# Kernel optimization log

Hardware: AMD Instinct MI355X
Metric: run time of the kernel (lower is better)

The kernel has to match this reference:

```python
import jax, jax.numpy as jnp
import numpy as np

# sigmas (defaults from the module)
VAR_0, VAR_A, VAR_B = 1.0, 1.0, 0.0

def V_phi(a, b, c):
    # default id_phi: (a, b, c) -> b, where Sigma = [[a, b], [b, c]]
    return b


def setup_inputs() -> dict:
    key = jax.random.key(0)
    kx, ky = jax.random.split(key)
    B, T, D = 128, 1024, 64
    dt = 1.0 / (T - 1)
    scale = np.sqrt(dt / D).astype(np.float32)
    # Brownian-like paths: increments ~ N(0, dt/D) so quadratic variation is O(1)
    # and the multiplicative kernel recurrence stays numerically bounded.
    X = jnp.cumsum(jax.random.normal(kx, (B, T, D), jnp.float32) * scale, axis=1)
    Y = jnp.cumsum(jax.random.normal(ky, (B, T, D), jnp.float32) * scale, axis=1)
    return {"X": X, "Y": Y}


def _kernel_same(dd):
    # dd: (b, T-1) = <dX_t, dX_t> / dt ; returns Kxx: (b, T)
    def step(k, d_t):
        k_new = k + (VAR_A * V_phi(k, k, k) + VAR_B) * d_t
        return k_new, k_new
    k0 = jnp.full((dd.shape[0],), VAR_0, dd.dtype)
    _, ks = jax.lax.scan(step, k0, dd.T)           # ks: (T-1, b)
    return jnp.concatenate([k0[None, :], ks], axis=0).T  # (b, T)


def reference(X, Y):
    bx, T, d = X.shape
    by = Y.shape[0]
    interval = jnp.linspace(0.0, 1.0, T).astype(X.dtype)
    dt = jnp.diff(interval)                         # (T-1,)
    dX = jnp.diff(X, axis=1)                        # (bx, T-1, d)
    dY = jnp.diff(Y, axis=1)                        # (by, T-1, d)

    dXdX = (dX * dX).sum(-1) / dt                   # (bx, T-1)
    dYdY = (dY * dY).sum(-1) / dt                   # (by, T-1)
    dXdY = jnp.einsum('itd,jtd->ijt', dX, dY) / dt  # (bx, by, T-1)

    Kxx = _kernel_same(dXdX)                        # (bx, T)
    Kyy = _kernel_same(dYdY)                        # (by, T)

    def step(k, inp):
        kxx_t, kyy_t, dxy_t = inp                   # (bx,), (by,), (bx, by)
        k_new = k + (VAR_A * V_phi(kxx_t[:, None], k, kyy_t[None, :]) + VAR_B) * dxy_t
        return k_new, k_new

    k0 = jnp.full((bx, by), VAR_0, X.dtype)
    xs = (Kxx[:, :-1].T, Kyy[:, :-1].T, jnp.moveaxis(dXdY, 2, 0))
    _, ks = jax.lax.scan(step, k0, xs)              # (T-1, bx, by)
    K = jnp.concatenate([k0[None], ks], axis=0)     # (T, bx, by)
    return jnp.moveaxis(K, 0, 2)                    # (bx, by, T)
```

## Files before the change

### kernel.cpp

```cpp
#include <hip/hip_runtime.h>
#include <hip/hip_bf16.h>

typedef __attribute__((ext_vector_type(8))) short short8;
typedef __attribute__((ext_vector_type(4))) float floatx4;

constexpr int BX    = 128;
constexpr int TT    = 1024;
constexpr int DDIM  = 64;
constexpr int NPAIR = BX * BX;
constexpr int LCH   = 16;
constexpr int NCH   = TT / LCH;
constexpr float DT_INV = 1023.0f;

__device__ __forceinline__ int sidxE(int row, int k) {
    return row * 64 + ((((k >> 3) ^ (row & 7)) << 3) | (k & 7));
}

__device__ __forceinline__ ushort f2bf(float f) {
    uint u = __builtin_bit_cast(uint, f);
    u += 0x7fffu + ((u >> 16) & 1u);
    return (ushort)(u >> 16);
}

__device__ __forceinline__ void cvt_store(ushort* hiP, ushort* loP, const float* v) {
    uint hw[4], lw[4];
#pragma unroll
    for (int p = 0; p < 4; ++p) {
        const __hip_bfloat162 h = __float22bfloat162_rn(make_float2(v[2 * p], v[2 * p + 1]));
        const float r0 = v[2 * p]     - __bfloat162float(h.x);
        const float r1 = v[2 * p + 1] - __bfloat162float(h.y);
        const __hip_bfloat162 l = __float22bfloat162_rn(make_float2(r0, r1));
        hw[p] = (uint)__bfloat16_as_ushort(h.x) | ((uint)__bfloat16_as_ushort(h.y) << 16);
        lw[p] = (uint)__bfloat16_as_ushort(l.x) | ((uint)__bfloat16_as_ushort(l.y) << 16);
    }
    *(uint4*)hiP = make_uint4(hw[0], hw[1], hw[2], hw[3]);
    *(uint4*)loP = make_uint4(lw[0], lw[1], lw[2], lw[3]);
}

__device__ __forceinline__ void ld8(const float* p, float* dst) {
    const float4 a = *(const float4*)p;
    const float4 b = *(const float4*)(p + 4);
    dst[0] = a.x; dst[1] = a.y; dst[2] = a.z; dst[3] = a.w;
    dst[4] = b.x; dst[5] = b.y; dst[6] = b.z; dst[7] = b.w;
}

template<int WP>
__global__ __launch_bounds__(256, 4) void zchunk_kernel(const float* __restrict__ X,
                                                        const float* __restrict__ Y,
                                                        float* __restrict__ dst,
                                                        float* __restrict__ P)
{
    __shared__ __align__(16) ushort smXhi[2][32 * 64], smXlo[2][32 * 64];
    __shared__ __align__(16) ushort smYhi[2][32 * 64], smYlo[2][32 * 64];

    const int L    = (int)blockIdx.x;
    const int tile = (L >> 3) & 15;
    const int cz   = ((L >> 7) << 3) | (L & 7);
    const int i0 = (tile & 3) * 32;
    const int j0 = (tile >> 2) * 32;
    const int t0 = cz * LCH;
    const int tid  = (int)threadIdx.x;
    const int lane = tid & 63, w = tid >> 6, quad = lane >> 4, l15 = lane & 15;
    const int wr = w >> 1, wc = w & 1;

    const int srow = tid >> 3;
    const int sseg = tid & 7;
    const float* xp = X + (size_t)(i0 + srow) * TT * DDIM + sseg * 8;
    const float* yp = Y + (size_t)(j0 + srow) * TT * DDIM + sseg * 8;

    float cx[8], cy[8];
    float rx[2][8], ry[2][8];
    {
        const int sa = (t0 == 0) ? 0 : (t0 - 1);
        float pvx[8], pvy[8], d[8];
        ld8(xp + (size_t)t0 * DDIM, cx);
        ld8(yp + (size_t)t0 * DDIM, cy);
        ld8(xp + (size_t)sa * DDIM, pvx);
        ld8(yp + (size_t)sa * DDIM, pvy);
        ld8(xp + (size_t)(t0 + 1) * DDIM, rx[1]);
        ld8(yp + (size_t)(t0 + 1) * DDIM, ry[1]);

#pragma unroll
        for (int k = 0; k < 8; ++k) d[k] = cx[k] - pvx[k];
        cvt_store(&smXhi[0][sidxE(srow, sseg * 8)], &smXlo[0][sidxE(srow, sseg * 8)], d);
#pragma unroll
        for (int k = 0; k < 8; ++k) d[k] = cy[k] - pvy[k];
        cvt_store(&smYhi[0][sidxE(srow, sseg * 8)], &smYlo[0][sidxE(srow, sseg * 8)], d);
    }

    float cum[4];
    uint  histP[4][8];
#pragma unroll
    for (int r = 0; r < 4; ++r) cum[r] = 1.f;

    __syncthreads();

#pragma unroll
    for (int h = 0; h < LCH; ++h) {
        const int cur = h & 1;

        if (h + 2 < LCH) {
            const size_t u = (size_t)(t0 + h + 2) * DDIM;
            ld8(xp + u, rx[h & 1]); ld8(yp + u, ry[h & 1]);
        }

        short8 aHi[2], aLo[2];
#pragma unroll
        for (int kk = 0; kk < 2; ++kk) {
            const int e = sidxE(wr * 16 + l15, kk * 32 + quad * 8);
            aHi[kk] = *(const short8*)&smXhi[cur][e];
            aLo[kk] = *(const short8*)&smXlo[cur][e];
        }

        floatx4 acc = {0.f, 0.f, 0.f, 0.f};
#pragma unroll
        for (int kk = 0; kk < 2; ++kk) {
            const int e = sidxE(wc * 16 + l15, kk * 32 + quad * 8);
            const short8 bHi = *(const short8*)&smYhi[cur][e];
            const short8 bLo = *(const short8*)&smYlo[cur][e];
            acc = __builtin_amdgcn_mfma_f32_16x16x32_bf16(aLo[kk], bHi, acc, 0, 0, 0);
            acc = __builtin_amdgcn_mfma_f32_16x16x32_bf16(aHi[kk], bLo, acc, 0, 0, 0);
            acc = __builtin_amdgcn_mfma_f32_16x16x32_bf16(aHi[kk], bHi, acc, 0, 0, 0);
        }
#pragma unroll
        for (int r = 0; r < 4; ++r) {
            cum[r] *= fmaf(acc[r], DT_INV, 1.f);
            const uint hb = (uint)f2bf(cum[r]);
            if ((h & 1) == 0) histP[r][h >> 1] = hb;
            else              histP[r][h >> 1] |= (hb << 16);
        }

        if (h + 1 < LCH) {
            const int nsel = (h + 1) & 1;
            float d[8];
#pragma unroll
            for (int k = 0; k < 8; ++k) d[k] = rx[nsel][k] - cx[k];
            cvt_store(&smXhi[cur ^ 1][sidxE(srow, sseg * 8)], &smXlo[cur ^ 1][sidxE(srow, sseg * 8)], d);
#pragma unroll
            for (int k = 0; k < 8; ++k) d[k] = ry[nsel][k] - cy[k];
            cvt_store(&smYhi[cur ^ 1][sidxE(srow, sseg * 8)], &smYlo[cur ^ 1][sidxE(srow, sseg * 8)], d);
#pragma unroll
            for (int k = 0; k < 8; ++k) { cx[k] = rx[nsel][k]; cy[k] = ry[nsel][k]; }
            __syncthreads();
        }
    }

#pragma unroll
    for (int r = 0; r < 4; ++r) {
        const int pair = (i0 + wr * 16 + quad * 4 + r) * BX + (j0 + wc * 16 + l15);
        P[(size_t)cz * NPAIR + pair] = cum[r];
        float* o = WP ? (dst + ((size_t)cz * NPAIR + pair) * LCH)
                      : (dst + (size_t)pair * TT + t0);
#pragma unroll
        for (int q = 0; q < 4; ++q) {
            const uint u0 = histP[r][2 * q];
            const uint u1 = histP[r][2 * q + 1];
            *(float4*)(o + q * 4) = make_float4(
                __builtin_bit_cast(float, u0 << 16),
                __builtin_bit_cast(float, u0 & 0xffff0000u),
                __builtin_bit_cast(float, u1 << 16),
                __builtin_bit_cast(float, u1 & 0xffff0000u));
        }
    }
}

__global__ __launch_bounds__(256) void scanscale_w(float* __restrict__ out,
                                                   const float* __restrict__ W,
                                                   const float* __restrict__ P)
{
    __shared__ float pf[NCH][17];
    __shared__ float tot[16][17];

    const int p0  = (int)blockIdx.x * 16;
    const int tid = (int)threadIdx.x;
    const int p   = tid & 15;
    const int seg = tid >> 4;

    float v[4], e[4];
#pragma unroll
    for (int k = 0; k < 4; ++k)
        v[k] = P[(size_t)(seg * 4 + k) * NPAIR + p0 + p];
    e[0] = 1.f;
#pragma unroll
    for (int k = 1; k < 4; ++k) e[k] = e[k - 1] * v[k - 1];
    tot[seg][p] = e[3] * v[3];
    __syncthreads();

    float base = 1.f;
#pragma unroll
    for (int q = 0; q < 15; ++q)
        if (q < seg) base *= tot[q][p];
#pragma unroll
    for (int k = 0; k < 4; ++k)
        pf[seg * 4 + k][p] = base * e[k];
    __syncthreads();

    const int wv = tid >> 6;
    const int l  = tid & 63;
    const int pr = l >> 2;
    const int tq = l & 3;
    float* orow = out + (size_t)(p0 + pr) * TT + tq * 4;
#pragma unroll 2
    for (int k = 0; k < 16; ++k) {
        const int c = wv * 16 + k;
        const float4 w4 = *(const float4*)(W + ((size_t)c * NPAIR + p0 + pr) * LCH + tq * 4);
        const float f = pf[c][pr];
        *(float4*)(orow + (size_t)c * LCH) =
            make_float4(w4.x * f, w4.y * f, w4.z * f, w4.w * f);
    }
}

__global__ __launch_bounds__(256) void scanscale_kernel(float* __restrict__ out,
                                                        const float* __restrict__ P)
{
    __shared__ float pf[16][NCH];
    const int p0  = (int)blockIdx.x * 16;
    const int tid = (int)threadIdx.x;

    if (tid < 16) {
        const int p = p0 + tid;
        float run = 1.f;
#pragma unroll 4
        for (int c = 0; c < NCH; ++c) {
            pf[tid][c] = run;
            run *= P[(size_t)c * NPAIR + p];
        }
    }
    __syncthreads();

    const int pp  = tid >> 4;
    const int col = tid & 15;
    float* row = out + (size_t)(p0 + pp) * TT;
#pragma unroll
    for (int seg = 0; seg < 16; ++seg) {
        const int t = seg * 64 + col * 4;
        const float f = pf[pp][t >> 4];
        float4 v = *(float4*)(row + t);
        v.x *= f; v.y *= f; v.z *= f; v.w *= f;
        *(float4*)(row + t) = v;
    }
}

extern "C" void kernel_launch(void* const* d_in, const int* in_sizes, int n_in,
                              void* d_out, int out_size, void* d_ws, size_t ws_size,
                              hipStream_t stream)
{
    const float* X = (const float*)d_in[0];
    const float* Y = (const float*)d_in[1];
    float* out = (float*)d_out;
    float* P   = (float*)d_ws;
    float* W   = (float*)d_ws + (size_t)NCH * NPAIR;

    const size_t need = ((size_t)NCH * NPAIR + (size_t)NPAIR * TT) * sizeof(float);
    if (ws_size >= need) {
        zchunk_kernel<1><<<dim3(1024), 256, 0, stream>>>(X, Y, W, P);
        scanscale_w<<<dim3(NPAIR / 16), 256, 0, stream>>>(out, W, P);
    } else {
        zchunk_kernel<0><<<dim3(1024), 256, 0, stream>>>(X, Y, out, P);
        scanscale_kernel<<<dim3(NPAIR / 16), 256, 0, stream>>>(out, P);
    }
}
```

Baseline: 176.3 us.

## Replace chunk-history workspace with recompute pass seeded by scanned chunk prefixes

The first pass now computes only the per-chunk products of the recurrence and writes them to a small buffer. A standalone scan kernel turns those into exclusive prefix products. A second pass uses 32-step chunks, recomputes the recurrence starting from the matching prefix, and writes final values straight to the output. This drops the full-size intermediate history buffer, which had to be written and then read back before scaling. The cost is running the MFMA recurrence twice, plus a third launch and lower occupancy in the second pass.

```diff
diff --git a/kernel.cpp b/kernel.cpp
--- a/kernel.cpp
+++ b/kernel.cpp
@@ -8,8 +8,8 @@
 constexpr int TT    = 1024;
 constexpr int DDIM  = 64;
 constexpr int NPAIR = BX * BX;
-constexpr int LCH   = 16;
-constexpr int NCH   = TT / LCH;
+constexpr int FCH   = 16;
+constexpr int NFCH  = TT / FCH;
 constexpr float DT_INV = 1023.0f;
 
 __device__ __forceinline__ int sidxE(int row, int k) {
@@ -44,12 +44,13 @@
     dst[4] = b.x; dst[5] = b.y; dst[6] = b.z; dst[7] = b.w;
 }
 
-template<int WP>
-__global__ __launch_bounds__(256, 4) void zchunk_kernel(const float* __restrict__ X,
-                                                        const float* __restrict__ Y,
-                                                        float* __restrict__ dst,
-                                                        float* __restrict__ P)
+template<int PASS>
+__global__ __launch_bounds__(256, (PASS == 1) ? 4 : 2)
+void zpass_kernel(const float* __restrict__ X, const float* __restrict__ Y,
+                  float* __restrict__ out, float* __restrict__ P)
 {
+    constexpr int STEPS = (PASS == 1) ? 16 : 32;
+
     __shared__ __align__(16) ushort smXhi[2][32 * 64], smXlo[2][32 * 64];
     __shared__ __align__(16) ushort smYhi[2][32 * 64], smYlo[2][32 * 64];
 
@@ -58,10 +59,21 @@
     const int cz   = ((L >> 7) << 3) | (L & 7);
     const int i0 = (tile & 3) * 32;
     const int j0 = (tile >> 2) * 32;
-    const int t0 = cz * LCH;
+    const int t0 = cz * STEPS;
     const int tid  = (int)threadIdx.x;
     const int lane = tid & 63, w = tid >> 6, quad = lane >> 4, l15 = lane & 15;
     const int wr = w >> 1, wc = w & 1;
+    const int pbase = (i0 + wr * 16 + quad * 4) * BX + (j0 + wc * 16 + l15);
+
+    float cum[4];
+    if (PASS == 2) {
+#pragma unroll
+        for (int r = 0; r < 4; ++r)
+            cum[r] = P[(size_t)(cz * 2) * NPAIR + pbase + r * BX];
+    } else {
+#pragma unroll
+        for (int r = 0; r < 4; ++r) cum[r] = 1.f;
+    }
 
     const int srow = tid >> 3;
     const int sseg = tid & 7;
@@ -88,18 +100,15 @@
         cvt_store(&smYhi[0][sidxE(srow, sseg * 8)], &smYlo[0][sidxE(srow, sseg * 8)], d);
     }
 
-    float cum[4];
-    uint  histP[4][8];
-#pragma unroll
-    for (int r = 0; r < 4; ++r) cum[r] = 1.f;
+    uint histP[4][STEPS / 2];
 
     __syncthreads();
 
 #pragma unroll
-    for (int h = 0; h < LCH; ++h) {
+    for (int h = 0; h < STEPS; ++h) {
         const int cur = h & 1;
 
-        if (h + 2 < LCH) {
+        if (h + 2 < STEPS) {
             const size_t u = (size_t)(t0 + h + 2) * DDIM;
             ld8(xp + u, rx[h & 1]); ld8(yp + u, ry[h & 1]);
         }
@@ -125,12 +134,14 @@
 #pragma unroll
         for (int r = 0; r < 4; ++r) {
             cum[r] *= fmaf(acc[r], DT_INV, 1.f);
-            const uint hb = (uint)f2bf(cum[r]);
-            if ((h & 1) == 0) histP[r][h >> 1] = hb;
-            else              histP[r][h >> 1] |= (hb << 16);
-        }
-
-        if (h + 1 < LCH) {
+            if (PASS == 2) {
+                const uint hb = (uint)f2bf(cum[r]);
+                if ((h & 1) == 0) histP[r][h >> 1] = hb;
+                else              histP[r][h >> 1] |= (hb << 16);
+            }
+        }
+
+        if (h + 1 < STEPS) {
             const int nsel = (h + 1) & 1;
             float d[8];
 #pragma unroll
@@ -145,99 +156,40 @@
         }
     }
 
-#pragma unroll
-    for (int r = 0; r < 4; ++r) {
-        const int pair = (i0 + wr * 16 + quad * 4 + r) * BX + (j0 + wc * 16 + l15);
-        P[(size_t)cz * NPAIR + pair] = cum[r];
-        float* o = WP ? (dst + ((size_t)cz * NPAIR + pair) * LCH)
-                      : (dst + (size_t)pair * TT + t0);
-#pragma unroll
-        for (int q = 0; q < 4; ++q) {
-            const uint u0 = histP[r][2 * q];
-            const uint u1 = histP[r][2 * q + 1];
-            *(float4*)(o + q * 4) = make_float4(
-                __builtin_bit_cast(float, u0 << 16),
-                __builtin_bit_cast(float, u0 & 0xffff0000u),
-                __builtin_bit_cast(float, u1 << 16),
-                __builtin_bit_cast(float, u1 & 0xffff0000u));
-        }
-    }
-}
-
-__global__ __launch_bounds__(256) void scanscale_w(float* __restrict__ out,
-                                                   const float* __restrict__ W,
-                                                   const float* __restrict__ P)
+    if (PASS == 1) {
+#pragma unroll
+        for (int r = 0; r < 4; ++r)
+            P[(size_t)cz * NPAIR + pbase + r * BX] = cum[r];
+    } else {
+#pragma unroll
+        for (int r = 0; r < 4; ++r) {
+            float* o = out + (size_t)(pbase + r * BX) * TT + t0;
+#pragma unroll
+            for (int q = 0; q < STEPS / 4; ++q) {
+                const uint u0 = histP[r][2 * q];
+                const uint u1 = histP[r][2 * q + 1];
+                *(float4*)(o + q * 4) = make_float4(
+                    __builtin_bit_cast(float, u0 << 16),
+                    __builtin_bit_cast(float, u0 & 0xffff0000u),
+                    __builtin_bit_cast(float, u1 << 16),
+                    __builtin_bit_cast(float, u1 & 0xffff0000u));
+            }
+        }
+    }
+}
+
+__global__ __launch_bounds__(64) void scan_kernel(float* __restrict__ P)
 {
-    __shared__ float pf[NCH][17];
-    __shared__ float tot[16][17];
-
-    const int p0  = (int)blockIdx.x * 16;
-    const int tid = (int)threadIdx.x;
-    const int p   = tid & 15;
-    const int seg = tid >> 4;
-
-    float v[4], e[4];
-#pragma unroll
-    for (int k = 0; k < 4; ++k)
-        v[k] = P[(size_t)(seg * 4 + k) * NPAIR + p0 + p];
-    e[0] = 1.f;
-#pragma unroll
-    for (int k = 1; k < 4; ++k) e[k] = e[k - 1] * v[k - 1];
-    tot[seg][p] = e[3] * v[3];
-    __syncthreads();
-
-    float base = 1.f;
-#pragma unroll
-    for (int q = 0; q < 15; ++q)
-        if (q < seg) base *= tot[q][p];
-#pragma unroll
-    for (int k = 0; k < 4; ++k)
-        pf[seg * 4 + k][p] = base * e[k];
-    __syncthreads();
-
-    const int wv = tid >> 6;
-    const int l  = tid & 63;
-    const int pr = l >> 2;
-    const int tq = l & 3;
-    float* orow = out + (size_t)(p0 + pr) * TT + tq * 4;
-#pragma unroll 2
-    for (int k = 0; k < 16; ++k) {
-        const int c = wv * 16 + k;
-        const float4 w4 = *(const float4*)(W + ((size_t)c * NPAIR + p0 + pr) * LCH + tq * 4);
-        const float f = pf[c][pr];
-        *(float4*)(orow + (size_t)c * LCH) =
-            make_float4(w4.x * f, w4.y * f, w4.z * f, w4.w * f);
-    }
-}
-
-__global__ __launch_bounds__(256) void scanscale_kernel(float* __restrict__ out,
-                                                        const float* __restrict__ P)
-{
-    __shared__ float pf[16][NCH];
-    const int p0  = (int)blockIdx.x * 16;
-    const int tid = (int)threadIdx.x;
-
-    if (tid < 16) {
-        const int p = p0 + tid;
-        float run = 1.f;
-#pragma unroll 4
-        for (int c = 0; c < NCH; ++c) {
-            pf[tid][c] = run;
-            run *= P[(size_t)c * NPAIR + p];
-        }
-    }
-    __syncthreads();
-
-    const int pp  = tid >> 4;
-    const int col = tid & 15;
-    float* row = out + (size_t)(p0 + pp) * TT;
-#pragma unroll
-    for (int seg = 0; seg < 16; ++seg) {
-        const int t = seg * 64 + col * 4;
-        const float f = pf[pp][t >> 4];
-        float4 v = *(float4*)(row + t);
-        v.x *= f; v.y *= f; v.z *= f; v.w *= f;
-        *(float4*)(row + t) = v;
+    const int p = (int)blockIdx.x * 64 + (int)threadIdx.x;
+    float v[NFCH];
+#pragma unroll
+    for (int c = 0; c < NFCH; ++c) v[c] = P[(size_t)c * NPAIR + p];
+    float run = 1.f;
+#pragma unroll
+    for (int c = 0; c < NFCH; ++c) {
+        const float t = v[c];
+        P[(size_t)c * NPAIR + p] = run;
+        run *= t;
     }
 }
 
@@ -249,14 +201,8 @@
     const float* Y = (const float*)d_in[1];
     float* out = (float*)d_out;
     float* P   = (float*)d_ws;
-    float* W   = (float*)d_ws + (size_t)NCH * NPAIR;
-
-    const size_t need = ((size_t)NCH * NPAIR + (size_t)NPAIR * TT) * sizeof(float);
-    if (ws_size >= need) {
-        zchunk_kernel<1><<<dim3(1024), 256, 0, stream>>>(X, Y, W, P);
-        scanscale_w<<<dim3(NPAIR / 16), 256, 0, stream>>>(out, W, P);
-    } else {
-        zchunk_kernel<0><<<dim3(1024), 256, 0, stream>>>(X, Y, out, P);
-        scanscale_kernel<<<dim3(NPAIR / 16), 256, 0, stream>>>(out, P);
-    }
-}
+
+    zpass_kernel<1><<<dim3(1024), 256, 0, stream>>>(X, Y, out, P);
+    scan_kernel<<<dim3(NPAIR / 64), 64, 0, stream>>>(P);
+    zpass_kernel<2><<<dim3(512), 256, 0, stream>>>(X, Y, out, P);
+}
```

New measurement: 211.6 us. 20.0% more time.
